# Optimization experiments

Measured on AMD Instinct MI355X. Metric: run time of the kernel, lower is better.

## Reference

```python
import jax, jax.numpy as jnp
import numpy as np

B, S, HID = 2, 1024, 2048
H, DK, DV = 8, 64, 128
TK, TV = H * DK, H * DV
K = 4                      # conv kernel size
GH = TV // 8               # generator hidden (reduction=8)
EPS = 1e-6


def setup_inputs() -> dict:
    key = jax.random.key(0)
    ks = jax.random.split(key, 10)
    sc = 0.02
    return {
        "hidden_states": jax.random.normal(ks[0], (B, S, HID), jnp.float32),
        "W_qkvabz": jax.random.normal(ks[1], (HID, TK + TK + TV + H + H + TV), jnp.float32) * sc,
        "A_log": jax.random.normal(ks[2], (H,), jnp.float32) * 0.5,
        "dt_bias": jax.random.normal(ks[3], (H,), jnp.float32) * 0.5,
        "conv_state": jax.random.normal(ks[4], (B, TV, K - 1), jnp.float32) * 0.1,
        "w1": jax.random.normal(ks[5], (HID, GH), jnp.float32) * sc,
        "w2": jax.random.normal(ks[6], (GH, TV * K), jnp.float32) * sc,
        "b2": jax.random.normal(ks[7], (TV * K,), jnp.float32) * sc,
        "init_state": jnp.zeros((B, H, DK, DV), jnp.float32),
        "o_norm_w": jnp.ones((DV,), jnp.float32),
        "W_o": jax.random.normal(ks[8], (TV, HID), jnp.float32) * sc,
    }


def _silu(x):
    return x * jax.nn.sigmoid(x)


def _l2norm(x):
    return x * jax.lax.rsqrt(jnp.sum(x * x, axis=-1, keepdims=True) + EPS)


def _dynamic_conv(v, hidden_states, conv_state, w1, w2, b2):
    # per-token depthwise conv kernels from a small MLP
    kernels = (_silu(hidden_states @ w1) @ w2 + b2).reshape(B, S, TV, K)
    # left-pad with cached state (conv_state: [B, TV, K-1] -> [B, K-1, TV])
    x_pad = jnp.concatenate([jnp.swapaxes(conv_state, 1, 2), v], axis=1)  # [B, S+K-1, TV]
    windows = jnp.stack([x_pad[:, j:j + S] for j in range(K)], axis=-1)   # [B, S, TV, K]
    return _silu(jnp.sum(windows * kernels, axis=-1))                      # [B, S, TV]


def _gated_delta_rule(q, k, v, g, beta, init_state):
    # q,k: [B,S,H,DK]; v: [B,S,H,DV]; g,beta: [B,S,H]; state: [B,H,DK,DV]
    q = _l2norm(q) * (DK ** -0.5)
    k = _l2norm(k)

    def step(h, inp):
        q_t, k_t, v_t, g_t, b_t = inp  # [B,H,DK],[B,H,DK],[B,H,DV],[B,H],[B,H]
        h = h * jnp.exp(g_t)[..., None, None]
        kv = jnp.einsum('bhk,bhkv->bhv', k_t, h)
        delta = (v_t - kv) * b_t[..., None]
        h = h + jnp.einsum('bhk,bhv->bhkv', k_t, delta)
        o_t = jnp.einsum('bhk,bhkv->bhv', q_t, h)
        return h, o_t

    xs = (jnp.moveaxis(q, 1, 0), jnp.moveaxis(k, 1, 0), jnp.moveaxis(v, 1, 0),
          jnp.moveaxis(g, 1, 0), jnp.moveaxis(beta, 1, 0))
    _, o = jax.lax.scan(step, init_state, xs)  # o: [S,B,H,DV]
    return jnp.moveaxis(o, 0, 1)               # [B,S,H,DV]


def reference(hidden_states, W_qkvabz, A_log, dt_bias, conv_state, w1, w2, b2,
              init_state, o_norm_w, W_o):
    qkvabz = hidden_states @ W_qkvabz
    q, k, v, a, beta, z = jnp.split(
        qkvabz, np.cumsum([TK, TK, TV, H, H])[:5].tolist(), axis=-1)

    q = _silu(q).reshape(B, S, H, DK)
    k = _silu(k).reshape(B, S, H, DK)

    v = _dynamic_conv(v, hidden_states, conv_state, w1, w2, b2)
    v = v.reshape(B, S, H, DV)

    g = -jnp.exp(A_log) * jax.nn.softplus(a + dt_bias)  # [B,S,H]
    beta = jax.nn.sigmoid(beta)                          # [B,S,H]

    o = _gated_delta_rule(q, k, v, g, beta, init_state)  # [B,S,H,DV]

    # gated RMSNorm: gate first, then normalize (fla GatedRMSNorm)
    z = z.reshape(B, S, H, DV)
    o = o * _silu(z)
    o = o * jax.lax.rsqrt(jnp.mean(o * o, axis=-1, keepdims=True) + EPS) * o_norm_w

    return o.reshape(B, S, TV) @ W_o
```

## Files before the change

kernel.cpp:

```cpp
#include <hip/hip_runtime.h>
#include <hip/hip_bf16.h>
#include <math.h>
#include <stdint.h>

#define BATCH 2
#define SEQ 1024
#define HIDDIM 2048
#define NH 8
#define DKD 64
#define DVD 128
#define TKD 512
#define TVD 1024
#define NCOL 3088
#define KSZ 4
#define NCHK 16

typedef __attribute__((ext_vector_type(8))) short bf16x8;
typedef __attribute__((ext_vector_type(4))) float f32x4;

__device__ __forceinline__ float sigm(float x){ return 1.f/(1.f+expf(-x)); }
__device__ __forceinline__ float siluf(float x){ return x/(1.f+expf(-x)); }
__device__ __forceinline__ float b2f(unsigned short u){
  union { unsigned int i; float f; } x; x.i = ((unsigned int)u) << 16; return x.f;
}
__device__ __forceinline__ unsigned short f2bu(float f){
  __hip_bfloat16 h = __float2bfloat16(f);
  return *(unsigned short*)&h;
}

__device__ __forceinline__ void glds16(const __hip_bfloat16* g, void* l) {
  __builtin_amdgcn_global_load_lds((const __attribute__((address_space(1))) void*)g,
                                   (__attribute__((address_space(3))) void*)l, 16, 0, 0);
}

__global__ __launch_bounds__(256) void prep_k(
    const float* __restrict__ Wqkvabz, const float* __restrict__ w1,
    const float* __restrict__ w2, const float* __restrict__ W_o,
    const float* __restrict__ hidden,
    __hip_bfloat16* __restrict__ Wcat, __hip_bfloat16* __restrict__ w2t,
    __hip_bfloat16* __restrict__ Wot, unsigned short* __restrict__ hidden_bf)
{
  __shared__ float tile[32][33];
  const int blk = blockIdx.x;
  const float* in; __hip_bfloat16* out; int R, C, bx, by;
  if (blk < 6400)      { in=Wqkvabz; out=Wcat; R=2048; C=3088; bx=blk%100; by=blk/100; }
  else if (blk < 6656) { int t=blk-6400; in=w1;  out=Wcat+(size_t)3200*2048; R=2048; C=128;  bx=t%4;   by=t/4; }
  else if (blk < 7168) { int t=blk-6656; in=w2;  out=w2t; R=128;  C=4096; bx=t%128; by=t/128; }
  else if (blk < 9216) { int t=blk-7168; in=W_o; out=Wot; R=1024; C=2048; bx=t%64;  by=t/64; }
  else {
    int i = (blk - 9216)*256 + threadIdx.x;
    float4 v = ((const float4*)hidden)[i];
    ushort4 o; o.x=f2bu(v.x); o.y=f2bu(v.y); o.z=f2bu(v.z); o.w=f2bu(v.w);
    ((ushort4*)hidden_bf)[i] = o;
    return;
  }
  const int tx = threadIdx.x & 31, ty = threadIdx.x >> 5;
  const int c = bx*32 + tx;
  #pragma unroll
  for (int i = 0; i < 4; ++i) {
    int r = by*32 + ty + i*8;
    tile[ty + i*8][tx] = (c < C) ? in[(size_t)r*C + c] : 0.f;
  }
  __syncthreads();
  #pragma unroll
  for (int i = 0; i < 4; ++i) {
    int orow = bx*32 + ty + i*8;
    int ocol = by*32 + tx;
    out[(size_t)orow*R + ocol] = __float2bfloat16(tile[tx][ty + i*8]);
  }
}

template<int EPI>
__global__ __launch_bounds__(256) void mgemm_k(
    const __hip_bfloat16* __restrict__ A,
    const __hip_bfloat16* __restrict__ Bt,
    const float* __restrict__ bias,
    float* __restrict__ Cf, __hip_bfloat16* __restrict__ Cb,
    int M, int N, int K, int nbx)
{
  __shared__ __hip_bfloat16 As[2][64*32];
  __shared__ __hip_bfloat16 Bs[2][128*32];
  const int tid = threadIdx.x;
  const int w = tid >> 6, l = tid & 63;
  const int wr = w >> 1, wc = w & 1;
  const int nwg = gridDim.x, q = nwg >> 3;
  const int swz = (blockIdx.x & 7)*q + (blockIdx.x >> 3);
  const int bx = swz % nbx, by = swz / nbx;
  const int row0 = by*64, col0 = bx*128;
  const int fr = l & 15, fq = l >> 4;

  f32x4 acc[2][4];
  #pragma unroll
  for (int m = 0; m < 2; ++m)
    #pragma unroll
    for (int n = 0; n < 4; ++n)
      acc[m][n] = (f32x4){0.f,0.f,0.f,0.f};

  const int ra = w*16 + (l >> 2);
  const int sg = (l & 3) ^ ((ra >> 1) & 3);
  const int ca = sg*8;

  const __hip_bfloat16* pA  = &A[(size_t)(row0 + ra)*K + ca];
  const __hip_bfloat16* pB0 = &Bt[(size_t)(col0 + ra)*K + ca];
  const __hip_bfloat16* pB1 = &Bt[(size_t)(col0 + ra + 64)*K + ca];

  glds16(pA,       (char*)&As[0][0] + w*1024);
  glds16(pB0,      (char*)&Bs[0][0] + w*1024);
  glds16(pB1,      (char*)&Bs[0][0] + 4096 + w*1024);
  if (K > 32) {
    glds16(pA  + 32, (char*)&As[1][0] + w*1024);
    glds16(pB0 + 32, (char*)&Bs[1][0] + w*1024);
    glds16(pB1 + 32, (char*)&Bs[1][0] + 4096 + w*1024);
  }

  int cur = 0;
  for (int k0 = 0; k0 < K; k0 += 32) {
    if (k0 + 32 < K) asm volatile("s_waitcnt vmcnt(3)" ::: "memory");
    else             asm volatile("s_waitcnt vmcnt(0)" ::: "memory");
    __builtin_amdgcn_s_barrier();

    bf16x8 af[2], bfv[4];
    #pragma unroll
    for (int m = 0; m < 2; ++m) {
      const int rw = wr*32 + m*16 + fr;
      af[m] = *(const bf16x8*)&As[cur][rw*32 + (fq ^ ((rw>>1)&3))*8];
    }
    #pragma unroll
    for (int n = 0; n < 4; ++n) {
      const int rw = wc*64 + n*16 + fr;
      bfv[n] = *(const bf16x8*)&Bs[cur][rw*32 + (fq ^ ((rw>>1)&3))*8];
    }
    #pragma unroll
    for (int m = 0; m < 2; ++m)
      #pragma unroll
      for (int n = 0; n < 4; ++n)
        acc[m][n] = __builtin_amdgcn_mfma_f32_16x16x32_bf16(af[m], bfv[n], acc[m][n], 0, 0, 0);

    __builtin_amdgcn_s_barrier();
    if (k0 + 64 < K) {
      glds16(pA  + k0 + 64, (char*)&As[cur][0] + w*1024);
      glds16(pB0 + k0 + 64, (char*)&Bs[cur][0] + w*1024);
      glds16(pB1 + k0 + 64, (char*)&Bs[cur][0] + 4096 + w*1024);
    }
    cur ^= 1;
  }

  #pragma unroll
  for (int n = 0; n < 4; ++n) {
    const int ccol = col0 + wc*64 + n*16 + fr;
    #pragma unroll
    for (int m = 0; m < 2; ++m) {
      #pragma unroll
      for (int r = 0; r < 4; ++r) {
        const int crow = row0 + wr*32 + m*16 + fq*4 + r;
        float v = acc[m][n][r];
        if (EPI == 0) {
          Cf[(size_t)crow*N + ccol] = v;
        } else if (EPI == 2) {
          Cb[(size_t)crow*N + ccol] = __float2bfloat16(v + bias[ccol]);
        } else {
          if (ccol < NCOL)       Cf[(size_t)crow*NCOL + ccol] = v;
          else if (ccol >= 3200) Cb[(size_t)crow*128 + (ccol - 3200)] = __float2bfloat16(siluf(v));
        }
      }
    }
  }
}

__global__ __launch_bounds__(256) void ac_k(const float* __restrict__ qkvabz,
    const float* __restrict__ A_log, const float* __restrict__ dt_bias,
    const __hip_bfloat16* __restrict__ kern, const float* __restrict__ conv_state,
    float* __restrict__ kn, unsigned short* __restrict__ qnb,
    unsigned short* __restrict__ knb,
    float* __restrict__ g, float* __restrict__ beta, float* __restrict__ vconv)
{
  if (blockIdx.x < 4096) {
    int gid = blockIdx.x*4 + (threadIdx.x >> 6);
    int lane = threadIdx.x & 63;
    int row = gid >> 3; int h = gid & 7;
    const float* base = qkvabz + (size_t)row * NCOL;
    float qv = base[h*64 + lane];
    float kv = base[TKD + h*64 + lane];
    float sq = siluf(qv), sk = siluf(kv);
    float ssq = sq*sq, ssk = sk*sk;
    #pragma unroll
    for (int o = 32; o; o >>= 1) { ssq += __shfl_xor(ssq, o); ssk += __shfl_xor(ssk, o); }
    float qn_v = sq * rsqrtf(ssq + 1e-6f) * 0.125f;
    float kn_v = sk * rsqrtf(ssk + 1e-6f);
    size_t idx = (size_t)row*TKD + h*64 + lane;
    kn[idx]  = kn_v;
    qnb[idx] = f2bu(qn_v);
    knb[idx] = f2bu(kn_v);
    if (lane == 0) {
      float av = base[2048 + h] + dt_bias[h];
      float sp = fmaxf(av, 0.f) + log1pf(expf(-fabsf(av)));
      g[(size_t)row*NH + h] = -expf(A_log[h]) * sp;
      float bv = base[2056 + h];
      beta[(size_t)row*NH + h] = sigm(bv);
    }
  } else {
    int idx = (blockIdx.x - 4096)*256 + threadIdx.x;
    int c = idx & (TVD-1);
    int bs = idx >> 10;
    int s = bs & (SEQ-1); int b = bs >> 10;
    ushort4 kf = *(const ushort4*)&kern[(size_t)idx * 4];
    float kj[4] = { b2f(kf.x), b2f(kf.y), b2f(kf.z), b2f(kf.w) };
    float acc = 0.f;
    #pragma unroll
    for (int j = 0; j < 4; ++j) {
      int i = s + j;
      float xv = (i < 3) ? conv_state[((size_t)b*TVD + c)*3 + i]
                         : qkvabz[((size_t)(b*SEQ + (i-3)))*NCOL + TKD*2 + c];
      acc = fmaf(xv, kj[j], acc);
    }
    vconv[idx] = siluf(acc);
  }
}

__global__ __launch_bounds__(256) void chunkA_k(const float* __restrict__ kn,
   const unsigned short* __restrict__ knb,
   const float* __restrict__ vconv, const float* __restrict__ gb,
   const float* __restrict__ bb, float* __restrict__ Gcbuf,
   float* __restrict__ Dbuf, float* __restrict__ Bvec,
   unsigned short* __restrict__ UvT, unsigned short* __restrict__ WnTb)
{
  const int blk = blockIdx.x;
  const int bh = blk >> 4, c = blk & 15;
  const int b = bh >> 3, h = bh & 7;
  const int tid = threadIdx.x;
  const int w = tid >> 6, l = tid & 63;
  const int fr = l & 15, fq = l >> 4;
  const int row0 = b*SEQ + c*64;

  __shared__ unsigned short Kb[64*72];
  __shared__ float Xv[64][132];
  __shared__ float Xw[64][68];
  __shared__ float AK[64][68];
  __shared__ float Gsh[64], Bsh[64];

  #pragma unroll
  for (int j = 0; j < 2; ++j) {
    int lin = tid + j*256; int t = lin >> 3, dq = (lin & 7)*8;
    *(uint4*)&Kb[t*72+dq] = *(const uint4*)&knb[(size_t)(row0+t)*TKD + h*64 + dq];
  }
  #pragma unroll
  for (int i = 0; i < 8; ++i) {
    int lin = tid + i*256; int t = lin >> 5, v4 = (lin & 31)*4;
    float4 vv = *(const float4*)&vconv[(size_t)(row0+t)*TVD + h*128 + v4];
    Xv[t][v4]=vv.x; Xv[t][v4+1]=vv.y; Xv[t][v4+2]=vv.z; Xv[t][v4+3]=vv.w;
  }
  if (tid < 64) {
    float gv = gb[(size_t)(row0+tid)*NH + h];
    #pragma unroll
    for (int o = 1; o < 64; o <<= 1) {
      float oth = __shfl_up(gv, o);
      if (tid >= o) gv += oth;
    }
    Gsh[tid] = gv;
    Bsh[tid] = bb[(size_t)(row0+tid)*NH + h];
    Gcbuf[(size_t)blk*64 + tid] = gv;
  }
  __syncthreads();

  {
    f32x4 accS[4];
    #pragma unroll
    for (int n = 0; n < 4; ++n) accS[n] = (f32x4){0.f,0.f,0.f,0.f};
    #pragma unroll
    for (int k0 = 0; k0 < 2; ++k0) {
      bf16x8 a = *(const bf16x8*)&Kb[(w*16+fr)*72 + k0*32 + fq*8];
      #pragma unroll
      for (int n = 0; n < 4; ++n) {
        bf16x8 bb2 = *(const bf16x8*)&Kb[(n*16+fr)*72 + k0*32 + fq*8];
        accS[n] = __builtin_amdgcn_mfma_f32_16x16x32_bf16(a, bb2, accS[n], 0, 0, 0);
      }
    }
    #pragma unroll
    for (int n = 0; n < 4; ++n)
      #pragma unroll
      for (int r = 0; r < 4; ++r) {
        int t = w*16 + fq*4 + r, s = n*16 + fr;
        AK[t][s] = (s < t) ? Bsh[t]*expf(Gsh[t]-Gsh[s])*accS[n][r] : 0.f;
      }
  }
  #pragma unroll
  for (int i = 0; i < 4; ++i) {
    int lin = tid + i*256; int t = lin >> 4, d4 = (lin & 15)*4;
    float4 kv = *(const float4*)&kn[(size_t)(row0+t)*TKD + h*64 + d4];
    float f = Bsh[t]*expf(Gsh[t]);
    Xw[t][d4+0]=f*kv.x; Xw[t][d4+1]=f*kv.y; Xw[t][d4+2]=f*kv.z; Xw[t][d4+3]=f*kv.w;
  }
  __syncthreads();

  if (tid < 192) {
    float x[64];
    if (tid < 128) {
      #pragma unroll
      for (int t = 0; t < 64; ++t) x[t] = Bsh[t]*Xv[t][tid];
    } else {
      #pragma unroll
      for (int t = 0; t < 64; ++t) x[t] = Xw[t][tid-128];
    }
    #pragma unroll
    for (int t = 1; t < 64; ++t) {
      float a0=0.f, a1=0.f, a2=0.f, a3=0.f;
      #pragma unroll
      for (int s4 = 0; s4 < (t+3)/4; ++s4) {
        float4 av = *(const float4*)&AK[t][s4*4];
        a0 = fmaf(av.x, x[s4*4+0], a0);
        a1 = fmaf(av.y, x[s4*4+1], a1);
        a2 = fmaf(av.z, x[s4*4+2], a2);
        a3 = fmaf(av.w, x[s4*4+3], a3);
      }
      x[t] -= (a0+a1)+(a2+a3);
    }
    if (tid < 128) {
      #pragma unroll
      for (int t = 0; t < 64; ++t) Xv[t][tid] = x[t];
    } else {
      #pragma unroll
      for (int t = 0; t < 64; ++t) Xw[t][tid-128] = x[t];
    }
  }
  __syncthreads();

  const float Gtot = Gsh[63];
  #pragma unroll
  for (int i = 0; i < 4; ++i) {
    int lin = tid + i*256; int t = lin >> 4, d4 = (lin & 15)*4;
    float4 kv = *(const float4*)&kn[(size_t)(row0+t)*TKD + h*64 + d4];
    float f = expf(Gtot - Gsh[t]);
    AK[t][d4+0]=f*kv.x; AK[t][d4+1]=f*kv.y; AK[t][d4+2]=f*kv.z; AK[t][d4+3]=f*kv.w;
  }
  __syncthreads();

  {
    const int d1b = (tid >> 4)*4, d2b = (tid & 15)*4;
    float dacc[4][4] = {};
    #pragma unroll 8
    for (int t = 0; t < 64; ++t) {
      float4 kw = *(const float4*)&AK[t][d1b];
      float4 wv = *(const float4*)&Xw[t][d2b];
      float kwa[4] = {kw.x,kw.y,kw.z,kw.w};
      float wva[4] = {wv.x,wv.y,wv.z,wv.w};
      #pragma unroll
      for (int i = 0; i < 4; ++i)
        #pragma unroll
        for (int j = 0; j < 4; ++j)
          dacc[i][j] = fmaf(kwa[i], wva[j], dacc[i][j]);
    }
    const float eG = expf(Gtot);
    #pragma unroll
    for (int i = 0; i < 4; ++i) {
      float vals[4];
      #pragma unroll
      for (int j = 0; j < 4; ++j) {
        float v = -dacc[i][j];
        if (d1b + i == d2b + j) v += eG;
        vals[j] = v;
      }
      *(float4*)&Dbuf[(size_t)blk*4096 + (d1b+i)*64 + d2b] =
        make_float4(vals[0],vals[1],vals[2],vals[3]);
    }
  }
  {
    const int d1b = (tid >> 4)*4, vb = (tid & 15)*8;
    float bacc[4][8] = {};
    #pragma unroll 4
    for (int t = 0; t < 64; ++t) {
      float4 kw = *(const float4*)&AK[t][d1b];
      float4 u0 = *(const float4*)&Xv[t][vb];
      float4 u1 = *(const float4*)&Xv[t][vb+4];
      float kwa[4] = {kw.x,kw.y,kw.z,kw.w};
      float ua[8] = {u0.x,u0.y,u0.z,u0.w,u1.x,u1.y,u1.z,u1.w};
      #pragma unroll
      for (int i = 0; i < 4; ++i)
        #pragma unroll
        for (int j = 0; j < 8; ++j)
          bacc[i][j] = fmaf(kwa[i], ua[j], bacc[i][j]);
    }
    #pragma unroll
    for (int i = 0; i < 4; ++i) {
      *(float4*)&Bvec[(size_t)blk*8192 + (d1b+i)*128 + vb] =
        make_float4(bacc[i][0],bacc[i][1],bacc[i][2],bacc[i][3]);
      *(float4*)&Bvec[(size_t)blk*8192 + (d1b+i)*128 + vb + 4] =
        make_float4(bacc[i][4],bacc[i][5],bacc[i][6],bacc[i][7]);
    }
  }

  {
    #pragma unroll
    for (int i = 0; i < 32; ++i) {
      int v = w*32 + i;
      UvT[(size_t)blk*8192 + v*64 + l] = f2bu(Xv[l][v]);
    }
    #pragma unroll
    for (int i = 0; i < 16; ++i) {
      int d = w*16 + i;
      WnTb[(size_t)blk*4096 + d*64 + l] = f2bu(-Xw[l][d]);
    }
  }
}

__global__ __launch_bounds__(256) void chunkB2_k(const float* __restrict__ Dbuf,
   const float* __restrict__ Bvec, const float* __restrict__ init,
   unsigned short* __restrict__ HcT)
{
  const int blk = blockIdx.x;
  const int bh = blk >> 3, grp = blk & 7;
  const int v0 = grp*16;
  const int tid = threadIdx.x;
  const int v = tid & 15;
  const int d1b = (tid >> 4) * 4;
  __shared__ float DT[64][68];
  __shared__ float bsh[64][17];
  __shared__ float hsh[64][17];

  float hreg[4];
  #pragma unroll
  for (int j = 0; j < 4; ++j) {
    hreg[j] = init[((size_t)bh*64 + d1b + j)*128 + v0 + v];
    hsh[d1b + j][v] = hreg[j];
  }
  float Dreg[16], breg[4];
  {
    const float* Dp = Dbuf + (size_t)(bh*16)*4096;
    const float* bp = Bvec + (size_t)(bh*16)*8192;
    #pragma unroll
    for (int i = 0; i < 16; ++i) Dreg[i] = Dp[tid + i*256];
    #pragma unroll
    for (int i = 0; i < 4; ++i)  breg[i] = bp[(size_t)((tid>>4) + i*16)*128 + v0 + v];
  }
  #pragma unroll
  for (int i = 0; i < 16; ++i) {
    int cell = tid + i*256; DT[cell & 63][cell >> 6] = Dreg[i];
  }
  #pragma unroll
  for (int i = 0; i < 4; ++i) bsh[(tid>>4) + i*16][v] = breg[i];
  __syncthreads();

  for (int c = 0; c < 16; ++c) {
    if (c < 15) {
      const float* Dn = Dbuf + (size_t)(bh*16 + c + 1)*4096;
      const float* bn = Bvec + (size_t)(bh*16 + c + 1)*8192;
      #pragma unroll
      for (int i = 0; i < 16; ++i) Dreg[i] = Dn[tid + i*256];
      #pragma unroll
      for (int i = 0; i < 4; ++i)  breg[i] = bn[(size_t)((tid>>4) + i*16)*128 + v0 + v];
    }
    #pragma unroll
    for (int j = 0; j < 4; ++j)
      HcT[(size_t)(bh*16 + c)*8192 + (size_t)(v0+v)*64 + d1b + j] = f2bu(hreg[j]);
    float nh[4];
    #pragma unroll
    for (int j = 0; j < 4; ++j) nh[j] = bsh[d1b + j][v];
    #pragma unroll 8
    for (int d2 = 0; d2 < 64; ++d2) {
      float hv = hsh[d2][v];
      float4 dv = *(const float4*)&DT[d2][d1b];
      nh[0] = fmaf(dv.x, hv, nh[0]);
      nh[1] = fmaf(dv.y, hv, nh[1]);
      nh[2] = fmaf(dv.z, hv, nh[2]);
      nh[3] = fmaf(dv.w, hv, nh[3]);
    }
    __syncthreads();
    #pragma unroll
    for (int j = 0; j < 4; ++j) { hreg[j] = nh[j]; hsh[d1b + j][v] = nh[j]; }
    if (c < 15) {
      #pragma unroll
      for (int i = 0; i < 16; ++i) {
        int cell = tid + i*256; DT[cell & 63][cell >> 6] = Dreg[i];
      }
      #pragma unroll
      for (int i = 0; i < 4; ++i) bsh[(tid>>4) + i*16][v] = breg[i];
    }
    __syncthreads();
  }
}

__global__ __launch_bounds__(256) void chunkC_k(
   const unsigned short* __restrict__ qnb, const unsigned short* __restrict__ knb,
   const unsigned short* __restrict__ UvT, const unsigned short* __restrict__ WnTb,
   const float* __restrict__ Gcbuf, const unsigned short* __restrict__ HcT,
   float* __restrict__ oattn)
{
  const int blk = blockIdx.x; const int bh = blk >> 4, c = blk & 15;
  const int b = bh >> 3, h = bh & 7;
  const int row0 = b*SEQ + c*64;
  const int tid = threadIdx.x;
  const int w = tid >> 6, l = tid & 63;
  const int fr = l & 15, fq = l >> 4;

  __shared__ unsigned short Qs[64*72];
  __shared__ unsigned short Ks[64*72];
  __shared__ unsigned short Ws[64*72];
  __shared__ unsigned short hT[128*72];
  __shared__ unsigned short UT[128*72];
  __shared__ unsigned short Ss[64*72];
  __shared__ float Gsh[64], Esh[64];

  #pragma unroll
  for (int j = 0; j < 2; ++j) {
    int lin = tid + j*256; int t = lin >> 3, dq = (lin & 7)*8;
    *(uint4*)&Qs[t*72+dq] = *(const uint4*)&qnb[(size_t)(row0+t)*TKD + h*64 + dq];
    *(uint4*)&Ks[t*72+dq] = *(const uint4*)&knb[(size_t)(row0+t)*TKD + h*64 + dq];
    *(uint4*)&Ws[t*72+dq] = *(const uint4*)&WnTb[(size_t)blk*4096 + t*64 + dq];
  }
  #pragma unroll
  for (int j = 0; j < 4; ++j) {
    int lin = tid + j*256; int v = lin >> 3, dq = (lin & 7)*8;
    *(uint4*)&hT[v*72+dq] = *(const uint4*)&HcT[(size_t)blk*8192 + (size_t)v*64 + dq];
    *(uint4*)&UT[v*72+dq] = *(const uint4*)&UvT[(size_t)blk*8192 + (size_t)v*64 + dq];
  }
  if (tid < 64) { float g = Gcbuf[(size_t)blk*64 + tid]; Gsh[tid] = g; Esh[tid] = expf(g); }
  __syncthreads();

  f32x4 accS[4];
  #pragma unroll
  for (int n = 0; n < 4; ++n) accS[n] = (f32x4){0.f,0.f,0.f,0.f};
  #pragma unroll
  for (int k0 = 0; k0 < 2; ++k0) {
    bf16x8 a = *(const bf16x8*)&Qs[(w*16+fr)*72 + k0*32 + fq*8];
    #pragma unroll
    for (int n = 0; n < 4; ++n) {
      bf16x8 bb = *(const bf16x8*)&Ks[(n*16+fr)*72 + k0*32 + fq*8];
      accS[n] = __builtin_amdgcn_mfma_f32_16x16x32_bf16(a, bb, accS[n], 0, 0, 0);
    }
  }
  #pragma unroll
  for (int n = 0; n < 4; ++n)
    #pragma unroll
    for (int r = 0; r < 4; ++r) {
      int t = w*16 + fq*4 + r, s = n*16 + fr;
      float val = (s <= t) ? expf(Gsh[t]-Gsh[s]) * accS[n][r] : 0.f;
      Ss[t*72 + s] = f2bu(val);
    }

  f32x4 accQ[4];
  #pragma unroll
  for (int n = 0; n < 4; ++n) {
    #pragma unroll
    for (int r = 0; r < 4; ++r) {
      int t = w*16 + fq*4 + r, d = n*16 + fr;
      accQ[n][r] = Esh[t] * b2f(Qs[t*72 + d]);
    }
    #pragma unroll
    for (int k0 = 0; k0 < 2; ++k0) {
      bf16x8 a = *(const bf16x8*)&Ss[(w*16+fr)*72 + k0*32 + fq*8];
      bf16x8 bb = *(const bf16x8*)&Ws[(n*16+fr)*72 + k0*32 + fq*8];
      accQ[n] = __builtin_amdgcn_mfma_f32_16x16x32_bf16(a, bb, accQ[n], 0, 0, 0);
    }
  }
  __syncthreads();

  #pragma unroll
  for (int n = 0; n < 4; ++n)
    #pragma unroll
    for (int r = 0; r < 4; ++r) {
      int t = w*16 + fq*4 + r, d = n*16 + fr;
      Ks[t*72 + d] = f2bu(accQ[n][r]);
    }

  #pragma unroll
  for (int n = 0; n < 8; ++n) {
    f32x4 acc = (f32x4){0.f,0.f,0.f,0.f};
    #pragma unroll
    for (int k0 = 0; k0 < 2; ++k0) {
      bf16x8 a1 = *(const bf16x8*)&Ks[(w*16+fr)*72 + k0*32 + fq*8];
      bf16x8 b1 = *(const bf16x8*)&hT[(n*16+fr)*72 + k0*32 + fq*8];
      acc = __builtin_amdgcn_mfma_f32_16x16x32_bf16(a1, b1, acc, 0, 0, 0);
      bf16x8 a2 = *(const bf16x8*)&Ss[(w*16+fr)*72 + k0*32 + fq*8];
      bf16x8 b2v = *(const bf16x8*)&UT[(n*16+fr)*72 + k0*32 + fq*8];
      acc = __builtin_amdgcn_mfma_f32_16x16x32_bf16(a2, b2v, acc, 0, 0, 0);
    }
    #pragma unroll
    for (int r = 0; r < 4; ++r) {
      int t = w*16 + fq*4 + r, v = n*16 + fr;
      oattn[(size_t)(row0+t)*TVD + h*128 + v] = acc[r];
    }
  }
}

__global__ __launch_bounds__(256) void norm_k(const float* __restrict__ oattn,
   const float* __restrict__ qkvabz, const float* __restrict__ onw,
   __hip_bfloat16* __restrict__ ofin)
{
  int gid = blockIdx.x*4 + (threadIdx.x >> 6);
  int lane = threadIdx.x & 63;
  int row = gid >> 3; int h = gid & 7;
  size_t ob = (size_t)row*TVD + h*128;
  float2 ov = *(const float2*)&oattn[ob + lane*2];
  float2 zv = *(const float2*)&qkvabz[(size_t)row*NCOL + 2064 + h*128 + lane*2];
  float g0 = ov.x * siluf(zv.x), g1 = ov.y * siluf(zv.y);
  float ss = g0*g0 + g1*g1;
  #pragma unroll
  for (int o = 32; o; o >>= 1) ss += __shfl_xor(ss, o);
  float r = rsqrtf(ss * (1.f/128.f) + 1e-6f);
  ofin[ob + lane*2]     = __float2bfloat16(g0 * r * onw[lane*2]);
  ofin[ob + lane*2 + 1] = __float2bfloat16(g1 * r * onw[lane*2+1]);
}

extern "C" void kernel_launch(void* const* d_in, const int* in_sizes, int n_in,
                              void* d_out, int out_size, void* d_ws, size_t ws_size,
                              hipStream_t stream) {
  const float* hidden     = (const float*)d_in[0];
  const float* Wqkvabz    = (const float*)d_in[1];
  const float* A_log      = (const float*)d_in[2];
  const float* dt_bias    = (const float*)d_in[3];
  const float* conv_state = (const float*)d_in[4];
  const float* w1         = (const float*)d_in[5];
  const float* w2         = (const float*)d_in[6];
  const float* b2         = (const float*)d_in[7];
  const float* init_state = (const float*)d_in[8];
  const float* o_norm_w   = (const float*)d_in[9];
  const float* W_o        = (const float*)d_in[10];
  float* out = (float*)d_out;

  float* ws = (float*)d_ws;
  float* qkvabz = ws;
  float* kern   = qkvabz + (size_t)6324224;
  float* qn     = kern   + (size_t)8388608;
  float* kn     = qn     + (size_t)1048576;
  float* gbuf   = kn     + (size_t)1048576;
  float* bbuf   = gbuf   + (size_t)16384;
  float* vconv  = bbuf   + (size_t)16384;
  float* bfpool = vconv  + (size_t)2097152;
  __hip_bfloat16* hidden_bf = (__hip_bfloat16*)bfpool;
  __hip_bfloat16* w1t   = hidden_bf + (size_t)4194304;
  __hip_bfloat16* w2t   = w1t + (size_t)262144;
  __hip_bfloat16* Wot   = w2t + (size_t)524288;
  __hip_bfloat16* x1sb  = Wot + (size_t)2097152;
  __hip_bfloat16* ofinb = x1sb + (size_t)262144;
  float* Gcbuf  = (float*)(ofinb + (size_t)2097152);
  __hip_bfloat16* Wcat   = (__hip_bfloat16*)kern;
  __hip_bfloat16* kernbf = (__hip_bfloat16*)kern;
  float* oattn  = kern;
  float* Dbuf   = kern + (size_t)2097152;
  float* Bvec   = kern + (size_t)3145728;
  unsigned short* UvTb  = (unsigned short*)(kern + (size_t)5242880);
  unsigned short* WnTbb = (unsigned short*)(kern + (size_t)6291456);
  unsigned short* qnb   = (unsigned short*)(kern + (size_t)6815744);
  unsigned short* knb   = (unsigned short*)(kern + (size_t)7340032);
  unsigned short* HcTb  = (unsigned short*)vconv;

  dim3 blk(256);
  prep_k<<<13312, blk, 0, stream>>>(Wqkvabz, w1, w2, W_o, hidden,
                                    Wcat, w2t, Wot, (unsigned short*)hidden_bf);
  mgemm_k<3><<<dim3(832),  blk, 0, stream>>>(hidden_bf, Wcat, nullptr, qkvabz, x1sb, 2048, 3328, 2048, 26);
  mgemm_k<2><<<dim3(1024), blk, 0, stream>>>(x1sb, w2t, b2, nullptr, kernbf, 2048, 4096, 128, 32);
  ac_k<<<12288, blk, 0, stream>>>(qkvabz, A_log, dt_bias, kernbf, conv_state,
                                  kn, qnb, knb, gbuf, bbuf, vconv);
  chunkA_k<<<256, blk, 0, stream>>>(kn, knb, vconv, gbuf, bbuf, Gcbuf, Dbuf, Bvec, UvTb, WnTbb);
  chunkB2_k<<<128, blk, 0, stream>>>(Dbuf, Bvec, init_state, HcTb);
  chunkC_k<<<256, blk, 0, stream>>>(qnb, knb, UvTb, WnTbb, Gcbuf, HcTb, oattn);
  norm_k<<<4096, blk, 0, stream>>>(oattn, qkvabz, o_norm_w, ofinb);
  mgemm_k<0><<<dim3(512),  blk, 0, stream>>>(ofinb, Wot, nullptr, out, nullptr, 2048, 2048, 1024, 16);
}
```

Baseline: 180.8 us.

## Fuse gated RMSNorm into chunk output kernel, store z in bf16, triple-buffer GEMM

The gated RMSNorm is folded into the chunk output kernel. Each wave now computes per-row sums of squares through 16-lane shuffles and writes the normalized bf16 output directly. This removes the separate norm kernel launch and the fp32 oattn write and re-read. The first GEMM epilogue now writes the z gate as bf16 into a spare buffer, which cuts z read traffic. Separately, the MFMA GEMM goes from double to triple-buffered LDS prefetch with deeper vmcnt waits, which hides more load latency at the cost of more LDS and lower occupancy.

```diff
diff --git a/kernel.cpp b/kernel.cpp
--- a/kernel.cpp
+++ b/kernel.cpp
@@ -76,10 +76,11 @@
     const __hip_bfloat16* __restrict__ Bt,
     const float* __restrict__ bias,
     float* __restrict__ Cf, __hip_bfloat16* __restrict__ Cb,
+    unsigned short* __restrict__ Zb,
     int M, int N, int K, int nbx)
 {
-  __shared__ __hip_bfloat16 As[2][64*32];
-  __shared__ __hip_bfloat16 Bs[2][128*32];
+  __shared__ __hip_bfloat16 As[3][64*32];
+  __shared__ __hip_bfloat16 Bs[3][128*32];
   const int tid = threadIdx.x;
   const int w = tid >> 6, l = tid & 63;
   const int wr = w >> 1, wc = w & 1;
@@ -112,11 +113,18 @@
     glds16(pB0 + 32, (char*)&Bs[1][0] + w*1024);
     glds16(pB1 + 32, (char*)&Bs[1][0] + 4096 + w*1024);
   }
+  if (K > 64) {
+    glds16(pA  + 64, (char*)&As[2][0] + w*1024);
+    glds16(pB0 + 64, (char*)&Bs[2][0] + w*1024);
+    glds16(pB1 + 64, (char*)&Bs[2][0] + 4096 + w*1024);
+  }
 
   int cur = 0;
   for (int k0 = 0; k0 < K; k0 += 32) {
-    if (k0 + 32 < K) asm volatile("s_waitcnt vmcnt(3)" ::: "memory");
-    else             asm volatile("s_waitcnt vmcnt(0)" ::: "memory");
+    const int ahead = (K - k0)/32 - 1;
+    if (ahead >= 2)      asm volatile("s_waitcnt vmcnt(6)" ::: "memory");
+    else if (ahead == 1) asm volatile("s_waitcnt vmcnt(3)" ::: "memory");
+    else                 asm volatile("s_waitcnt vmcnt(0)" ::: "memory");
     __builtin_amdgcn_s_barrier();
 
     bf16x8 af[2], bfv[4];
@@ -137,12 +145,12 @@
         acc[m][n] = __builtin_amdgcn_mfma_f32_16x16x32_bf16(af[m], bfv[n], acc[m][n], 0, 0, 0);
 
     __builtin_amdgcn_s_barrier();
-    if (k0 + 64 < K) {
-      glds16(pA  + k0 + 64, (char*)&As[cur][0] + w*1024);
-      glds16(pB0 + k0 + 64, (char*)&Bs[cur][0] + w*1024);
-      glds16(pB1 + k0 + 64, (char*)&Bs[cur][0] + 4096 + w*1024);
-    }
-    cur ^= 1;
+    if (k0 + 96 < K) {
+      glds16(pA  + k0 + 96, (char*)&As[cur][0] + w*1024);
+      glds16(pB0 + k0 + 96, (char*)&Bs[cur][0] + w*1024);
+      glds16(pB1 + k0 + 96, (char*)&Bs[cur][0] + 4096 + w*1024);
+    }
+    cur = (cur == 2) ? 0 : cur + 1;
   }
 
   #pragma unroll
@@ -159,7 +167,8 @@
         } else if (EPI == 2) {
           Cb[(size_t)crow*N + ccol] = __float2bfloat16(v + bias[ccol]);
         } else {
-          if (ccol < NCOL)       Cf[(size_t)crow*NCOL + ccol] = v;
+          if (ccol < 2064)       Cf[(size_t)crow*NCOL + ccol] = v;
+          else if (ccol < 3088)  Zb[(size_t)crow*1024 + (ccol - 2064)] = f2bu(v);
           else if (ccol >= 3200) Cb[(size_t)crow*128 + (ccol - 3200)] = __float2bfloat16(siluf(v));
         }
       }
@@ -482,7 +491,8 @@
    const unsigned short* __restrict__ qnb, const unsigned short* __restrict__ knb,
    const unsigned short* __restrict__ UvT, const unsigned short* __restrict__ WnTb,
    const float* __restrict__ Gcbuf, const unsigned short* __restrict__ HcT,
-   float* __restrict__ oattn)
+   const unsigned short* __restrict__ Zb, const float* __restrict__ onw,
+   __hip_bfloat16* __restrict__ ofin)
 {
   const int blk = blockIdx.x; const int bh = blk >> 4, c = blk & 15;
   const int b = bh >> 3, h = bh & 7;
@@ -561,6 +571,7 @@
       Ks[t*72 + d] = f2bu(accQ[n][r]);
     }
 
+  float og[8][4];
   #pragma unroll
   for (int n = 0; n < 8; ++n) {
     f32x4 acc = (f32x4){0.f,0.f,0.f,0.f};
@@ -574,30 +585,44 @@
       acc = __builtin_amdgcn_mfma_f32_16x16x32_bf16(a2, b2v, acc, 0, 0, 0);
     }
     #pragma unroll
+    for (int r = 0; r < 4; ++r) og[n][r] = acc[r];
+  }
+
+  float ss0 = 0.f, ss1 = 0.f, ss2 = 0.f, ss3 = 0.f;
+  #pragma unroll
+  for (int n = 0; n < 8; ++n) {
+    #pragma unroll
     for (int r = 0; r < 4; ++r) {
       int t = w*16 + fq*4 + r, v = n*16 + fr;
-      oattn[(size_t)(row0+t)*TVD + h*128 + v] = acc[r];
-    }
-  }
-}
-
-__global__ __launch_bounds__(256) void norm_k(const float* __restrict__ oattn,
-   const float* __restrict__ qkvabz, const float* __restrict__ onw,
-   __hip_bfloat16* __restrict__ ofin)
-{
-  int gid = blockIdx.x*4 + (threadIdx.x >> 6);
-  int lane = threadIdx.x & 63;
-  int row = gid >> 3; int h = gid & 7;
-  size_t ob = (size_t)row*TVD + h*128;
-  float2 ov = *(const float2*)&oattn[ob + lane*2];
-  float2 zv = *(const float2*)&qkvabz[(size_t)row*NCOL + 2064 + h*128 + lane*2];
-  float g0 = ov.x * siluf(zv.x), g1 = ov.y * siluf(zv.y);
-  float ss = g0*g0 + g1*g1;
-  #pragma unroll
-  for (int o = 32; o; o >>= 1) ss += __shfl_xor(ss, o);
-  float r = rsqrtf(ss * (1.f/128.f) + 1e-6f);
-  ofin[ob + lane*2]     = __float2bfloat16(g0 * r * onw[lane*2]);
-  ofin[ob + lane*2 + 1] = __float2bfloat16(g1 * r * onw[lane*2+1]);
+      float zf = b2f(Zb[(size_t)(row0+t)*1024 + h*128 + v]);
+      float g0 = og[n][r] * siluf(zf);
+      og[n][r] = g0;
+      float g2 = g0*g0;
+      if      (r == 0) ss0 += g2;
+      else if (r == 1) ss1 += g2;
+      else if (r == 2) ss2 += g2;
+      else             ss3 += g2;
+    }
+  }
+  #pragma unroll
+  for (int o = 1; o <= 8; o <<= 1) {
+    ss0 += __shfl_xor(ss0, o); ss1 += __shfl_xor(ss1, o);
+    ss2 += __shfl_xor(ss2, o); ss3 += __shfl_xor(ss3, o);
+  }
+  float rr[4];
+  rr[0] = rsqrtf(ss0*(1.f/128.f) + 1e-6f);
+  rr[1] = rsqrtf(ss1*(1.f/128.f) + 1e-6f);
+  rr[2] = rsqrtf(ss2*(1.f/128.f) + 1e-6f);
+  rr[3] = rsqrtf(ss3*(1.f/128.f) + 1e-6f);
+  #pragma unroll
+  for (int n = 0; n < 8; ++n) {
+    float ow = onw[n*16 + fr];
+    #pragma unroll
+    for (int r = 0; r < 4; ++r) {
+      int t = w*16 + fq*4 + r, v = n*16 + fr;
+      ofin[(size_t)(row0+t)*1024 + h*128 + v] = __float2bfloat16(og[n][r] * rr[r] * ow);
+    }
+  }
 }
 
 extern "C" void kernel_launch(void* const* d_in, const int* in_sizes, int n_in,
@@ -619,8 +644,8 @@
   float* ws = (float*)d_ws;
   float* qkvabz = ws;
   float* kern   = qkvabz + (size_t)6324224;
-  float* qn     = kern   + (size_t)8388608;
-  float* kn     = qn     + (size_t)1048576;
+  float* zspare = kern   + (size_t)8388608;
+  float* kn     = zspare + (size_t)1048576;
   float* gbuf   = kn     + (size_t)1048576;
   float* bbuf   = gbuf   + (size_t)16384;
   float* vconv  = bbuf   + (size_t)16384;
@@ -634,7 +659,6 @@
   float* Gcbuf  = (float*)(ofinb + (size_t)2097152);
   __hip_bfloat16* Wcat   = (__hip_bfloat16*)kern;
   __hip_bfloat16* kernbf = (__hip_bfloat16*)kern;
-  float* oattn  = kern;
   float* Dbuf   = kern + (size_t)2097152;
   float* Bvec   = kern + (size_t)3145728;
   unsigned short* UvTb  = (unsigned short*)(kern + (size_t)5242880);
@@ -642,17 +666,17 @@
   unsigned short* qnb   = (unsigned short*)(kern + (size_t)6815744);
   unsigned short* knb   = (unsigned short*)(kern + (size_t)7340032);
   unsigned short* HcTb  = (unsigned short*)vconv;
+  unsigned short* zb    = (unsigned short*)zspare;
 
   dim3 blk(256);
   prep_k<<<13312, blk, 0, stream>>>(Wqkvabz, w1, w2, W_o, hidden,
                                     Wcat, w2t, Wot, (unsigned short*)hidden_bf);
-  mgemm_k<3><<<dim3(832),  blk, 0, stream>>>(hidden_bf, Wcat, nullptr, qkvabz, x1sb, 2048, 3328, 2048, 26);
-  mgemm_k<2><<<dim3(1024), blk, 0, stream>>>(x1sb, w2t, b2, nullptr, kernbf, 2048, 4096, 128, 32);
+  mgemm_k<3><<<dim3(832),  blk, 0, stream>>>(hidden_bf, Wcat, nullptr, qkvabz, x1sb, zb, 2048, 3328, 2048, 26);
+  mgemm_k<2><<<dim3(1024), blk, 0, stream>>>(x1sb, w2t, b2, nullptr, kernbf, nullptr, 2048, 4096, 128, 32);
   ac_k<<<12288, blk, 0, stream>>>(qkvabz, A_log, dt_bias, kernbf, conv_state,
                                   kn, qnb, knb, gbuf, bbuf, vconv);
   chunkA_k<<<256, blk, 0, stream>>>(kn, knb, vconv, gbuf, bbuf, Gcbuf, Dbuf, Bvec, UvTb, WnTbb);
   chunkB2_k<<<128, blk, 0, stream>>>(Dbuf, Bvec, init_state, HcTb);
-  chunkC_k<<<256, blk, 0, stream>>>(qnb, knb, UvTb, WnTbb, Gcbuf, HcTb, oattn);
-  norm_k<<<4096, blk, 0, stream>>>(oattn, qkvabz, o_norm_w, ofinb);
-  mgemm_k<0><<<dim3(512),  blk, 0, stream>>>(ofinb, Wot, nullptr, out, nullptr, 2048, 2048, 1024, 16);
-}
+  chunkC_k<<<256, blk, 0, stream>>>(qnb, knb, UvTb, WnTbb, Gcbuf, HcTb, zb, o_norm_w, ofinb);
+  mgemm_k<0><<<dim3(512),  blk, 0, stream>>>(ofinb, Wot, nullptr, out, nullptr, nullptr, 2048, 2048, 1024, 16);
+}
```

Measured after the change: 179.1 us. About the same (-0.9%).
